# Performance work log

Hardware: AMD Instinct MI355X
Metric: run time of the kernel (lower is better)

## Reference

```python
import jax, jax.numpy as jnp
import numpy as np

LOC_SIZE, LOC_EMB = 100000, 256
TIM_SIZE, TIM_EMB = 48, 64
UID_SIZE, UID_EMB = 5000, 128
HID = 512
B, T = 64, 128
L_HIST, G = 1024, 4  # 256 history groups of size 4


def setup_inputs() -> dict:
    key = jax.random.key(0)
    ks = jax.random.split(key, 16)
    s = 0.02
    inp = {
        "loc": jax.random.randint(ks[0], (B, T), 0, LOC_SIZE),
        "tim": jax.random.randint(ks[1], (B, T), 0, TIM_SIZE),
        "input_lengths": jax.random.randint(ks[2], (B,), 1, T + 1),
        "history_loc": jax.random.randint(ks[3], (B, L_HIST), 0, LOC_SIZE),
        "history_tim": jax.random.randint(ks[4], (B, L_HIST), 0, TIM_SIZE),
        "history_uid": jax.random.randint(ks[5], (B, L_HIST), 0, UID_SIZE),
        "group_size": G,
        "emb_loc": jax.random.normal(ks[6], (LOC_SIZE, LOC_EMB), jnp.float32) * s,
        "emb_tim": jax.random.normal(ks[7], (TIM_SIZE, TIM_EMB), jnp.float32) * s,
        "emb_uid": jax.random.normal(ks[8], (UID_SIZE, UID_EMB), jnp.float32) * s,
        "W_attn": jax.random.normal(ks[9], (HID, LOC_EMB + TIM_EMB + UID_EMB), jnp.float32) * s,
        "b_attn": jnp.zeros((HID,), jnp.float32),
        "W_ih": jax.random.normal(ks[10], (3 * HID, LOC_EMB + TIM_EMB), jnp.float32) * s,
        "b_ih": jnp.zeros((3 * HID,), jnp.float32),
        "W_hh": jax.random.normal(ks[11], (3 * HID, HID), jnp.float32) * s,
        "b_hh": jnp.zeros((3 * HID,), jnp.float32),
        "W_final": jax.random.normal(ks[12], (UID_SIZE, 3 * HID), jnp.float32) * s,
        "b_final": jnp.zeros((UID_SIZE,), jnp.float32),
    }
    return inp


def _gru(x_seq, W_ih, b_ih, W_hh, b_hh):
    # x_seq: [T, B, Din] -> outputs [T, B, H], PyTorch gate order (r, z, n)
    H = W_hh.shape[1]
    gx = jnp.einsum("tbd,gd->tbg", x_seq, W_ih) + b_ih  # [T,B,3H]
    h0 = jnp.zeros((x_seq.shape[1], H), x_seq.dtype)

    def step(h, gx_t):
        gh = h @ W_hh.T + b_hh
        xr, xz, xn = jnp.split(gx_t, 3, axis=-1)
        hr, hz, hn = jnp.split(gh, 3, axis=-1)
        r = jax.nn.sigmoid(xr + hr)
        z = jax.nn.sigmoid(xz + hz)
        n = jnp.tanh(xn + r * hn)
        h_new = (1.0 - z) * n + z * h
        return h_new, h_new

    _, outs = jax.lax.scan(step, h0, gx)
    return outs  # [T,B,H]


def reference(loc, tim, input_lengths, history_loc, history_tim, history_uid,
              group_size, emb_loc, emb_tim, emb_uid, W_attn, b_attn,
              W_ih, b_ih, W_hh, b_hh, W_final, b_final):
    Bn, Tn = loc.shape
    # current-trajectory embeddings -> GRU (dropout is identity in eval)
    x = jnp.concatenate([emb_loc[loc], emb_tim[tim]], axis=-1)  # [B,T,Din]
    outs = _gru(jnp.swapaxes(x, 0, 1), W_ih, b_ih, W_hh, b_hh)  # [T,B,H]
    outs = jnp.swapaxes(outs, 0, 1)                              # [B,T,H]
    last = outs[jnp.arange(Bn), input_lengths - 1]               # [B,H]

    # history pooling: groups of size G; uid emb averaged within group,
    # loc/tim embeddings taken at each group's first element
    Gc = group_size
    n_groups = history_uid.shape[1] // Gc
    uid_h = emb_uid[history_uid].reshape(Bn, n_groups, Gc, -1).mean(axis=2)  # [B,N,Du]
    loc_h = emb_loc[history_loc[:, ::Gc]]                                    # [B,N,Dl]
    tim_h = emb_tim[history_tim[:, ::Gc]]                                    # [B,N,Dt]
    hist = jnp.concatenate([loc_h, tim_h, uid_h], axis=-1)
    hist = jnp.tanh(jnp.einsum("bnd,hd->bnh", hist, W_attn) + b_attn)        # [B,N,H]

    # 'dot' attention: replaces the nested python-loop scoring
    energies = jnp.einsum("bh,bnh->bn", last, hist)
    attn_w = jax.nn.softmax(energies, axis=-1)
    context = jnp.einsum("bn,bnh->bh", attn_w, hist)

    out = jnp.concatenate([last, context, last], axis=-1)  # [B,3H]
    y = out @ W_final.T + b_final                          # [B,U]
    # original assigns y (one row) into score[t] of shape [T,U] -> broadcast over T
    score = jnp.broadcast_to(y[:, None, :], (Bn, Tn, y.shape[-1]))
    return score
```

## Files before the change

### kernel.cpp

```cpp
#include <hip/hip_runtime.h>
#include <hip/hip_bf16.h>


typedef __attribute__((ext_vector_type(8))) short bf16x8;
typedef __attribute__((ext_vector_type(4))) float f32x4;
typedef __attribute__((ext_vector_type(4))) unsigned short u16x4;
typedef __attribute__((ext_vector_type(2))) unsigned long long u64x2;
typedef unsigned long long u64;

__device__ inline unsigned short f2bf(float x) {
  __hip_bfloat16 b = __float2bfloat16(x);
  return __builtin_bit_cast(unsigned short, b);
}
__device__ inline bf16x8 pack8(float4 a, float4 b) {
  bf16x8 w;
  w[0]=(short)f2bf(a.x); w[1]=(short)f2bf(a.y); w[2]=(short)f2bf(a.z); w[3]=(short)f2bf(a.w);
  w[4]=(short)f2bf(b.x); w[5]=(short)f2bf(b.y); w[6]=(short)f2bf(b.z); w[7]=(short)f2bf(b.w);
  return w;
}

__global__ __launch_bounds__(256)
void gemm_gx_f(const int* __restrict__ loc, const int* __restrict__ tim,
               const float* __restrict__ eloc, const float* __restrict__ etim,
               const float* __restrict__ W_ih, const float* __restrict__ b_ih,
               float* __restrict__ gx) {
  constexpr int LDR = 40, K = 320, N = 1536;
  __shared__ short Asl[128 * LDR];
  __shared__ short Bsl[128 * LDR];
  const int tid = threadIdx.x;
  const int lane = tid & 63, wid = tid >> 6;
  const int wr = wid >> 1, wc = wid & 1;
  const int m16 = lane & 15, g4 = lane >> 4;
  const int bm = blockIdx.y * 128, bn = blockIdx.x * 128;
  const int srow = tid >> 1, shalf = tid & 1;
  const int grow = bm + srow;
  const int t_ = grow >> 6, b_ = grow & 63;
  const float* aloc = eloc + (size_t)loc[b_ * 128 + t_] * 256 + (shalf << 4);
  const float* atim = etim + (size_t)tim[b_ * 128 + t_] * 64 + (shalf << 4);
  const float* bbase = W_ih + (size_t)(bn + srow) * K + (shalf << 4);
  float4 a0, a1, a2, a3, w0, w1, w2, w3;
  {
    a0 = ((const float4*)aloc)[0]; a1 = ((const float4*)aloc)[1];
    a2 = ((const float4*)aloc)[2]; a3 = ((const float4*)aloc)[3];
    w0 = ((const float4*)bbase)[0]; w1 = ((const float4*)bbase)[1];
    w2 = ((const float4*)bbase)[2]; w3 = ((const float4*)bbase)[3];
  }
  f32x4 acc[4][4] = {};
  for (int k0 = 0; k0 < K; k0 += 32) {
    short* arow = Asl + srow * LDR + (shalf << 4);
    *(bf16x8*)(arow)     = pack8(a0, a1);
    *(bf16x8*)(arow + 8) = pack8(a2, a3);
    short* brow = Bsl + srow * LDR + (shalf << 4);
    *(bf16x8*)(brow)     = pack8(w0, w1);
    *(bf16x8*)(brow + 8) = pack8(w2, w3);
    __syncthreads();
    if (k0 + 32 < K) {
      const int kn = k0 + 32;
      const float* ap = (kn < 256) ? (aloc + kn) : (atim + (kn - 256));
      a0 = ((const float4*)ap)[0]; a1 = ((const float4*)ap)[1];
      a2 = ((const float4*)ap)[2]; a3 = ((const float4*)ap)[3];
      const float* bp = bbase + kn;
      w0 = ((const float4*)bp)[0]; w1 = ((const float4*)bp)[1];
      w2 = ((const float4*)bp)[2]; w3 = ((const float4*)bp)[3];
    }
    bf16x8 af[4], bfr[4];
#pragma unroll
    for (int i = 0; i < 4; ++i) {
      af[i]  = *(const bf16x8*)(Asl + ((wr << 6) + (i << 4) + m16) * LDR + (g4 << 3));
      bfr[i] = *(const bf16x8*)(Bsl + ((wc << 6) + (i << 4) + m16) * LDR + (g4 << 3));
    }
#pragma unroll
    for (int i = 0; i < 4; ++i)
#pragma unroll
      for (int j = 0; j < 4; ++j)
        acc[i][j] = __builtin_amdgcn_mfma_f32_16x16x32_bf16(af[i], bfr[j], acc[i][j], 0, 0, 0);
    __syncthreads();
  }
#pragma unroll
  for (int i = 0; i < 4; ++i)
#pragma unroll
    for (int j = 0; j < 4; ++j) {
      const int col = bn + (wc << 6) + (j << 4) + m16;
      const float bv = b_ih[col];
#pragma unroll
      for (int q = 0; q < 4; ++q) {
        const int row = bm + (wr << 6) + (i << 4) + (g4 << 2) + q;
        gx[(size_t)row * N + col] = acc[i][j][q] + bv;
      }
    }
}

__global__ __launch_bounds__(256)
void gru_attn(const float* __restrict__ gx, const float* __restrict__ W_hh,
              const float* __restrict__ b_hh, const int* __restrict__ lens,
              short* __restrict__ h_bf, float* __restrict__ lastb,
              unsigned int* __restrict__ flags,
              const int* __restrict__ hloc, const int* __restrict__ htim,
              const int* __restrict__ huid,
              const float* __restrict__ eloc, const float* __restrict__ etim,
              const float* __restrict__ euid,
              const float* __restrict__ W_attn, const float* __restrict__ b_attn,
              float* __restrict__ histt, float* __restrict__ ctx) {
  __shared__ short smem[6 * 16 * 512];
  const int bid = blockIdx.x;
  const int tid = threadIdx.x;

  if (bid < 64) {
    if (tid >= 128) return;
    const int lane = tid & 63, tt = tid >> 6;
    const int c = bid >> 2, grp = bid & 3;
    const int j0 = (c << 5) + (tt << 4);
    const int b0 = grp << 4;
    const int m16 = lane & 15, g4 = lane >> 4;

    for (int gi = 0; gi < 3; ++gi) {
      const float* wg = W_hh + (size_t)(gi * 512 + j0) * 512;
      short* slab = smem + (((gi << 1) + tt) << 13);
      for (int r = 0; r < 16; ++r) {
        int k = lane << 3;
        const float4* src = (const float4*)(wg + (size_t)r * 512 + k);
        int off = ((r << 9) + k) ^ ((r & 7) << 3);
        *(bf16x8*)(slab + off) = pack8(src[0], src[1]);
      }
    }

    const int bcol = b0 + m16;
    const int jr = j0 + (g4 << 2);
    const f32x4 bhr = *(const f32x4*)&b_hh[jr];
    const f32x4 bhz = *(const f32x4*)&b_hh[512 + jr];
    const f32x4 bhn = *(const f32x4*)&b_hh[1024 + jr];
    const int lenb = lens[bcol];
    f32x4 hprev = {0.f, 0.f, 0.f, 0.f};

    unsigned int* gflags = flags + (grp << 9);
    unsigned int* ownflag = gflags + (((c << 1) + tt) << 4);

    for (int t = 0; t < 128; ++t) {
      const float* gxb = gx + ((size_t)t * 64 + bcol) * 1536;
      f32x4 gr = *(const f32x4*)(gxb + jr);
      f32x4 gz = *(const f32x4*)(gxb + 512 + jr);
      f32x4 gn = *(const f32x4*)(gxb + 1024 + jr);
      f32x4 ar = {0.f, 0.f, 0.f, 0.f}, az = ar, an = ar;
      if (t) {
        unsigned tgt = (unsigned)t;
        while (true) {
          unsigned f = tgt;
          if (lane < 32)
            f = __hip_atomic_load(gflags + (lane << 4), __ATOMIC_RELAXED, __HIP_MEMORY_SCOPE_AGENT);
          if (__all((int)(f >= tgt))) break;
        }
        asm volatile("" ::: "memory");

        const u64* hp = (const u64*)(h_bf + ((t & 1) << 15) + (size_t)bcol * 512 + (g4 << 3));
        u64 hu[32];
#pragma unroll
        for (int ks = 0; ks < 16; ++ks) {
          hu[2 * ks]     = __hip_atomic_load(hp + ks * 8,     __ATOMIC_RELAXED, __HIP_MEMORY_SCOPE_AGENT);
          hu[2 * ks + 1] = __hip_atomic_load(hp + ks * 8 + 1, __ATOMIC_RELAXED, __HIP_MEMORY_SCOPE_AGENT);
        }
#define GRU_MFMA(ks)                                                                 \
        {                                                                            \
          u64x2 p; p[0] = hu[2 * (ks)]; p[1] = hu[2 * (ks) + 1];                     \
          bf16x8 hf = __builtin_bit_cast(bf16x8, p);                                 \
          int off = ((m16 << 9) + ((ks) << 5) + (g4 << 3)) ^ ((m16 & 7) << 3);       \
          ar = __builtin_amdgcn_mfma_f32_16x16x32_bf16(*(const bf16x8*)(smem + ((0 + tt) << 13) + off), hf, ar, 0, 0, 0); \
          az = __builtin_amdgcn_mfma_f32_16x16x32_bf16(*(const bf16x8*)(smem + ((2 + tt) << 13) + off), hf, az, 0, 0, 0); \
          an = __builtin_amdgcn_mfma_f32_16x16x32_bf16(*(const bf16x8*)(smem + ((4 + tt) << 13) + off), hf, an, 0, 0, 0); \
        }
        GRU_MFMA(0)  GRU_MFMA(1)  GRU_MFMA(2)  GRU_MFMA(3)
        GRU_MFMA(4)  GRU_MFMA(5)  GRU_MFMA(6)  GRU_MFMA(7)
        GRU_MFMA(8)  GRU_MFMA(9)  GRU_MFMA(10) GRU_MFMA(11)
        GRU_MFMA(12) GRU_MFMA(13) GRU_MFMA(14) GRU_MFMA(15)
#undef GRU_MFMA
      }
      u16x4 hw;
#pragma unroll
      for (int q = 0; q < 4; ++q) {
        float r = 1.f / (1.f + __expf(-(gr[q] + ar[q] + bhr[q])));
        float z = 1.f / (1.f + __expf(-(gz[q] + az[q] + bhz[q])));
        float xn = gn[q] + r * (an[q] + bhn[q]);
        float n = 1.f - 2.f / (__expf(2.f * xn) + 1.f);
        float hv = (1.f - z) * n + z * hprev[q];
        hprev[q] = hv;
        hw[q] = f2bf(hv);
      }
      __hip_atomic_store((u64*)(h_bf + ((~t & 1) << 15) + (size_t)bcol * 512 + jr),
                         __builtin_bit_cast(u64, hw),
                         __ATOMIC_RELAXED, __HIP_MEMORY_SCOPE_AGENT);
      if (t == lenb - 1) {
        *(f32x4*)(lastb + (size_t)bcol * 512 + jr) = hprev;
      }
      if (t < 127) {
        asm volatile("s_waitcnt vmcnt(0)" ::: "memory");
        if (lane == 0)
          __hip_atomic_store(ownflag, (unsigned)(t + 1), __ATOMIC_RELAXED, __HIP_MEMORY_SCOPE_AGENT);
      }
    }
    asm volatile("s_waitcnt vmcnt(0)" ::: "memory");
    if (lane == 0)
      __hip_atomic_fetch_add(flags + 2064, 1u, __ATOMIC_RELEASE, __HIP_MEMORY_SCOPE_AGENT);
    return;
  }

  {
    constexpr int LDR = 40, K = 448, N = 512;
    short* Asl = smem;
    short* Bsl = smem + 128 * LDR;
    const int lane = tid & 63, wid = tid >> 6;
    const int wr = wid >> 1, wc = wid & 1;
    const int m16 = lane & 15, g4 = lane >> 4;
    const int srow = tid >> 1, shalf = tid & 1;
    for (int tile = bid - 64; tile < 512; tile += 128) {
      const int yt = tile >> 2, nt = tile & 3;
      const int bm = yt << 7, bn = nt << 7;
      f32x4 acc[4][4] = {};
      for (int k0 = 0; k0 < K; k0 += 32) {
        {
          const int grow = bm + srow;
          const int b = grow >> 8, n = grow & 255;
          const int base = b * 1024 + (n << 2);
          float4 f0, f1, f2, f3;
          if (k0 < 256) {
            const float* ap = eloc + (size_t)hloc[base] * 256 + k0 + (shalf << 4);
            f0 = ((const float4*)ap)[0]; f1 = ((const float4*)ap)[1];
            f2 = ((const float4*)ap)[2]; f3 = ((const float4*)ap)[3];
          } else if (k0 < 320) {
            const float* ap = etim + (size_t)htim[base] * 64 + (k0 - 256) + (shalf << 4);
            f0 = ((const float4*)ap)[0]; f1 = ((const float4*)ap)[1];
            f2 = ((const float4*)ap)[2]; f3 = ((const float4*)ap)[3];
          } else {
            const int cu = (k0 - 320) + (shalf << 4);
            const float4* u0 = (const float4*)(euid + (size_t)huid[base + 0] * 128 + cu);
            const float4* u1 = (const float4*)(euid + (size_t)huid[base + 1] * 128 + cu);
            const float4* u2 = (const float4*)(euid + (size_t)huid[base + 2] * 128 + cu);
            const float4* u3 = (const float4*)(euid + (size_t)huid[base + 3] * 128 + cu);
#define AVG4(idx, dst) { float4 a=u0[idx],b4=u1[idx],c4=u2[idx],d4=u3[idx];            \
            dst.x=0.25f*(a.x+b4.x+c4.x+d4.x); dst.y=0.25f*(a.y+b4.y+c4.y+d4.y);       \
            dst.z=0.25f*(a.z+b4.z+c4.z+d4.z); dst.w=0.25f*(a.w+b4.w+c4.w+d4.w); }
            AVG4(0, f0) AVG4(1, f1) AVG4(2, f2) AVG4(3, f3)
#undef AVG4
          }
          short* arow = Asl + srow * LDR + (shalf << 4);
          *(bf16x8*)(arow)     = pack8(f0, f1);
          *(bf16x8*)(arow + 8) = pack8(f2, f3);
          const float* bp = W_attn + (size_t)(bn + srow) * K + k0 + (shalf << 4);
          f0 = ((const float4*)bp)[0]; f1 = ((const float4*)bp)[1];
          f2 = ((const float4*)bp)[2]; f3 = ((const float4*)bp)[3];
          short* brow = Bsl + srow * LDR + (shalf << 4);
          *(bf16x8*)(brow)     = pack8(f0, f1);
          *(bf16x8*)(brow + 8) = pack8(f2, f3);
        }
        __syncthreads();
        bf16x8 af[4], bfr[4];
#pragma unroll
        for (int i = 0; i < 4; ++i) {
          af[i]  = *(const bf16x8*)(Asl + ((wr << 6) + (i << 4) + m16) * LDR + (g4 << 3));
          bfr[i] = *(const bf16x8*)(Bsl + ((wc << 6) + (i << 4) + m16) * LDR + (g4 << 3));
        }
#pragma unroll
        for (int i = 0; i < 4; ++i)
#pragma unroll
          for (int j = 0; j < 4; ++j)
            acc[i][j] = __builtin_amdgcn_mfma_f32_16x16x32_bf16(af[i], bfr[j], acc[i][j], 0, 0, 0);
        __syncthreads();
      }
#pragma unroll
      for (int i = 0; i < 4; ++i)
#pragma unroll
        for (int j = 0; j < 4; ++j) {
          const int col = bn + (wc << 6) + (j << 4) + m16;
          const float bv = b_attn[col];
#pragma unroll
          for (int q = 0; q < 4; ++q) {
            const int row = bm + (wr << 6) + (i << 4) + (g4 << 2) + q;
            histt[(size_t)row * N + col] = tanhf(acc[i][j][q] + bv);
          }
        }
    }
    asm volatile("s_waitcnt vmcnt(0)" ::: "memory");
    if (tid == 0)
      __hip_atomic_fetch_add(flags + 2048, 1u, __ATOMIC_RELEASE, __HIP_MEMORY_SCOPE_AGENT);
  }

  if (bid < 128) {
    while (true) {
      unsigned a = __hip_atomic_load(flags + 2048, __ATOMIC_RELAXED, __HIP_MEMORY_SCOPE_AGENT);
      unsigned g = __hip_atomic_load(flags + 2064, __ATOMIC_RELAXED, __HIP_MEMORY_SCOPE_AGENT);
      if (a >= 128u && g >= 128u) break;
      __builtin_amdgcn_s_sleep(2);
    }
    __builtin_amdgcn_fence(__ATOMIC_ACQUIRE, "agent");
    __syncthreads();
    const int b = bid - 64;
    float* ls  = (float*)smem;
    float* wv  = ls + 512;
    float* red = wv + 256;
    ((float2*)ls)[tid] = ((const float2*)(lastb + (size_t)b * 512))[tid];
    __syncthreads();
    const float* hb = histt + (size_t)b * 256 * 512;
    const float* hrow = hb + (size_t)tid * 512;
    float acc = 0.f;
    for (int k = 0; k < 512; k += 4) {
      float4 h4 = *(const float4*)(hrow + k);
      acc += ls[k] * h4.x + ls[k + 1] * h4.y + ls[k + 2] * h4.z + ls[k + 3] * h4.w;
    }
    red[tid] = acc;
    __syncthreads();
    for (int s = 128; s; s >>= 1) {
      if (tid < s) red[tid] = fmaxf(red[tid], red[tid + s]);
      __syncthreads();
    }
    float m = red[0];
    __syncthreads();
    float ex = expf(acc - m);
    wv[tid] = ex; red[tid] = ex;
    __syncthreads();
    for (int s = 128; s; s >>= 1) {
      if (tid < s) red[tid] += red[tid + s];
      __syncthreads();
    }
    float inv = 1.f / red[0];
    float c0 = 0.f, c1 = 0.f;
    for (int n = 0; n < 256; ++n) {
      float wn = wv[n];
      c0 += wn * hb[(size_t)n * 512 + tid];
      c1 += wn * hb[(size_t)n * 512 + tid + 256];
    }
    ctx[(size_t)b * 512 + tid]       = c0 * inv;
    ctx[(size_t)b * 512 + tid + 256] = c1 * inv;
  }
}

__global__ __launch_bounds__(256)
void final_gemm(const float* __restrict__ last, const float* __restrict__ ctx,
                const float* __restrict__ Wf, const float* __restrict__ bf,
                float* __restrict__ y) {
  __shared__ float s[64][132];
  const int tid = threadIdx.x;
  const int u0 = blockIdx.x << 3;
  const int ul = tid >> 6, b = tid & 63;
  float acc0 = 0.f, acc1 = 0.f;
  for (int kc = 0; kc < 12; ++kc) {
    __syncthreads();
    for (int i = tid; i < 2048; i += 256) {
      int rb = i >> 5, cc = (i & 31) << 2;
      int k = kc * 128 + cc;
      const float* src = (k < 512) ? (last + (size_t)rb * 512 + k)
                       : (k < 1024) ? (ctx + (size_t)rb * 512 + k - 512)
                                    : (last + (size_t)rb * 512 + k - 1024);
      *(float4*)&s[rb][cc] = *(const float4*)src;
    }
    __syncthreads();
#pragma unroll
    for (int uu = 0; uu < 2; ++uu) {
      int u = u0 + ul + uu * 4;
      const float* wrow = Wf + (size_t)u * 1536 + kc * 128;
      float a = 0.f;
#pragma unroll 8
      for (int c = 0; c < 128; c += 4) {
        float4 w4 = *(const float4*)(wrow + c);
        float4 s4 = *(const float4*)&s[b][c];
        a += w4.x * s4.x + w4.y * s4.y + w4.z * s4.z + w4.w * s4.w;
      }
      if (uu == 0) acc0 += a; else acc1 += a;
    }
  }
  int u = u0 + ul;
  y[(size_t)b * 5000 + u]     = acc0 + bf[u];
  y[(size_t)b * 5000 + u + 4] = acc1 + bf[u + 4];
}

__global__ void broadcast_y(const float* __restrict__ y, float* __restrict__ out) {
  int bt = blockIdx.x;
  const float4* src = (const float4*)(y + (size_t)(bt >> 7) * 5000);
  float4* dst = (float4*)(out + (size_t)bt * 5000);
  for (int i = threadIdx.x; i < 1250; i += 256) dst[i] = src[i];
}

extern "C" void kernel_launch(void* const* d_in, const int* in_sizes, int n_in,
                              void* d_out, int out_size, void* d_ws, size_t ws_size,
                              hipStream_t stream) {
  const int* loc  = (const int*)d_in[0];
  const int* tim  = (const int*)d_in[1];
  const int* lens = (const int*)d_in[2];
  const int* hloc = (const int*)d_in[3];
  const int* htim = (const int*)d_in[4];
  const int* huid = (const int*)d_in[5];
  const float* eloc    = (const float*)d_in[7];
  const float* etim    = (const float*)d_in[8];
  const float* euid    = (const float*)d_in[9];
  const float* W_attn  = (const float*)d_in[10];
  const float* b_attn  = (const float*)d_in[11];
  const float* W_ih    = (const float*)d_in[12];
  const float* b_ih    = (const float*)d_in[13];
  const float* W_hh    = (const float*)d_in[14];
  const float* b_hh    = (const float*)d_in[15];
  const float* W_final = (const float*)d_in[16];
  const float* b_final = (const float*)d_in[17];
  float* out = (float*)d_out;
  char* ws = (char*)d_ws;

  float* gx    = (float*)(ws + 0ull);
  float* histt = (float*)(ws + 50331648ull);
  float* lastb = (float*)(ws + 83886080ull);
  float* ctx   = (float*)(ws + 84017152ull);
  float* yv    = (float*)(ws + 84148224ull);
  short* h_bf  = (short*)(ws + 85428224ull);
  unsigned int* flags = (unsigned int*)(ws + 85559296ull);

  hipMemsetAsync(flags, 0, 12288, stream);
  gemm_gx_f<<<dim3(12, 64), 256, 0, stream>>>(loc, tim, eloc, etim, W_ih, b_ih, gx);

  gru_attn<<<192, 256, 0, stream>>>(gx, W_hh, b_hh, lens, h_bf, lastb, flags,
                                    hloc, htim, huid, eloc, etim, euid,
                                    W_attn, b_attn, histt, ctx);

  final_gemm<<<625, 256, 0, stream>>>(lastb, ctx, W_final, b_final, yv);
  broadcast_y<<<8192, 256, 0, stream>>>(yv, out);
}
```

Before: 672.4 us.

## Repartition GRU across 32 four-wave blocks and fold duplicated W_final columns

The recurrent GRU part now runs on 32 blocks of four waves instead of 64 blocks of two. Each block covers 64 hidden units, which cuts the number of cross-block flags polled per step from 32 to 8. The n-gate W_hh slice is kept in registers and the r/z slices in LDS, and waves in a block sync with __syncthreads before publishing the step flag. The history-attention blocks, while waiting, also precompute W_final[:, :512] + W_final[:, 1024:], since `last` appears twice in the concatenation. This lets final_gemm read a K of 1024 instead of 1536. The added block barrier per step and the extra register pressure could lengthen each serial step.

```diff
diff --git a/kernel.cpp b/kernel.cpp
--- a/kernel.cpp
+++ b/kernel.cpp
@@ -90,7 +90,7 @@
     }
 }
 
-__global__ __launch_bounds__(256)
+__global__ __launch_bounds__(256, 1)
 void gru_attn(const float* __restrict__ gx, const float* __restrict__ W_hh,
               const float* __restrict__ b_hh, const int* __restrict__ lens,
               short* __restrict__ h_bf, float* __restrict__ lastb,
@@ -100,27 +100,37 @@
               const float* __restrict__ eloc, const float* __restrict__ etim,
               const float* __restrict__ euid,
               const float* __restrict__ W_attn, const float* __restrict__ b_attn,
+              const float* __restrict__ Wf, float* __restrict__ Wfold,
               float* __restrict__ histt, float* __restrict__ ctx) {
-  __shared__ short smem[6 * 16 * 512];
+  __shared__ short smem[8 * 16 * 512];
   const int bid = blockIdx.x;
   const int tid = threadIdx.x;
 
-  if (bid < 64) {
-    if (tid >= 128) return;
-    const int lane = tid & 63, tt = tid >> 6;
+  if (bid < 32) {
+    const int lane = tid & 63, w = tid >> 6;
     const int c = bid >> 2, grp = bid & 3;
-    const int j0 = (c << 5) + (tt << 4);
+    const int j0 = (c << 6) + (w << 4);
     const int b0 = grp << 4;
     const int m16 = lane & 15, g4 = lane >> 4;
 
-    for (int gi = 0; gi < 3; ++gi) {
+    for (int gi = 0; gi < 2; ++gi) {
       const float* wg = W_hh + (size_t)(gi * 512 + j0) * 512;
-      short* slab = smem + (((gi << 1) + tt) << 13);
+      short* slab = smem + (((w << 1) + gi) << 13);
       for (int r = 0; r < 16; ++r) {
         int k = lane << 3;
         const float4* src = (const float4*)(wg + (size_t)r * 512 + k);
         int off = ((r << 9) + k) ^ ((r & 7) << 3);
         *(bf16x8*)(slab + off) = pack8(src[0], src[1]);
+      }
+    }
+    bf16x8 wn_[16];
+    {
+      const float* wnp = W_hh + (size_t)(1024 + j0 + m16) * 512 + (g4 << 3);
+#pragma unroll
+      for (int ks = 0; ks < 16; ++ks) {
+        float4 x0 = *(const float4*)(wnp + ks * 32);
+        float4 x1 = *(const float4*)(wnp + ks * 32 + 4);
+        wn_[ks] = pack8(x0, x1);
       }
     }
 
@@ -132,8 +142,8 @@
     const int lenb = lens[bcol];
     f32x4 hprev = {0.f, 0.f, 0.f, 0.f};
 
-    unsigned int* gflags = flags + (grp << 9);
-    unsigned int* ownflag = gflags + (((c << 1) + tt) << 4);
+    unsigned int* gflags = flags + (grp << 7);
+    unsigned int* ownflag = gflags + (c << 4);
 
     for (int t = 0; t < 128; ++t) {
       const float* gxb = gx + ((size_t)t * 64 + bcol) * 1536;
@@ -145,7 +155,7 @@
         unsigned tgt = (unsigned)t;
         while (true) {
           unsigned f = tgt;
-          if (lane < 32)
+          if (lane < 8)
             f = __hip_atomic_load(gflags + (lane << 4), __ATOMIC_RELAXED, __HIP_MEMORY_SCOPE_AGENT);
           if (__all((int)(f >= tgt))) break;
         }
@@ -163,9 +173,9 @@
           u64x2 p; p[0] = hu[2 * (ks)]; p[1] = hu[2 * (ks) + 1];                     \
           bf16x8 hf = __builtin_bit_cast(bf16x8, p);                                 \
           int off = ((m16 << 9) + ((ks) << 5) + (g4 << 3)) ^ ((m16 & 7) << 3);       \
-          ar = __builtin_amdgcn_mfma_f32_16x16x32_bf16(*(const bf16x8*)(smem + ((0 + tt) << 13) + off), hf, ar, 0, 0, 0); \
-          az = __builtin_amdgcn_mfma_f32_16x16x32_bf16(*(const bf16x8*)(smem + ((2 + tt) << 13) + off), hf, az, 0, 0, 0); \
-          an = __builtin_amdgcn_mfma_f32_16x16x32_bf16(*(const bf16x8*)(smem + ((4 + tt) << 13) + off), hf, an, 0, 0, 0); \
+          ar = __builtin_amdgcn_mfma_f32_16x16x32_bf16(*(const bf16x8*)(smem + ((w << 1) << 13) + off), hf, ar, 0, 0, 0);       \
+          az = __builtin_amdgcn_mfma_f32_16x16x32_bf16(*(const bf16x8*)(smem + (((w << 1) + 1) << 13) + off), hf, az, 0, 0, 0); \
+          an = __builtin_amdgcn_mfma_f32_16x16x32_bf16(wn_[ks], hf, an, 0, 0, 0);    \
         }
         GRU_MFMA(0)  GRU_MFMA(1)  GRU_MFMA(2)  GRU_MFMA(3)
         GRU_MFMA(4)  GRU_MFMA(5)  GRU_MFMA(6)  GRU_MFMA(7)
@@ -192,12 +202,14 @@
       }
       if (t < 127) {
         asm volatile("s_waitcnt vmcnt(0)" ::: "memory");
-        if (lane == 0)
+        __syncthreads();
+        if (tid == 0)
           __hip_atomic_store(ownflag, (unsigned)(t + 1), __ATOMIC_RELAXED, __HIP_MEMORY_SCOPE_AGENT);
       }
     }
     asm volatile("s_waitcnt vmcnt(0)" ::: "memory");
-    if (lane == 0)
+    __syncthreads();
+    if (tid == 0)
       __hip_atomic_fetch_add(flags + 2064, 1u, __ATOMIC_RELEASE, __HIP_MEMORY_SCOPE_AGENT);
     return;
   }
@@ -210,7 +222,7 @@
     const int wr = wid >> 1, wc = wid & 1;
     const int m16 = lane & 15, g4 = lane >> 4;
     const int srow = tid >> 1, shalf = tid & 1;
-    for (int tile = bid - 64; tile < 512; tile += 128) {
+    for (int tile = bid - 32; tile < 512; tile += 128) {
       const int yt = tile >> 2, nt = tile & 3;
       const int bm = yt << 7, bn = nt << 7;
       f32x4 acc[4][4] = {};
@@ -280,18 +292,28 @@
     asm volatile("s_waitcnt vmcnt(0)" ::: "memory");
     if (tid == 0)
       __hip_atomic_fetch_add(flags + 2048, 1u, __ATOMIC_RELEASE, __HIP_MEMORY_SCOPE_AGENT);
-  }
-
-  if (bid < 128) {
-    while (true) {
-      unsigned a = __hip_atomic_load(flags + 2048, __ATOMIC_RELAXED, __HIP_MEMORY_SCOPE_AGENT);
-      unsigned g = __hip_atomic_load(flags + 2064, __ATOMIC_RELAXED, __HIP_MEMORY_SCOPE_AGENT);
-      if (a >= 128u && g >= 128u) break;
-      __builtin_amdgcn_s_sleep(2);
-    }
+
+    for (int u = bid - 32; u < 5000; u += 128) {
+      const int cc = tid << 1;
+      float2 a = *(const float2*)(Wf + (size_t)u * 1536 + cc);
+      float2 b2 = *(const float2*)(Wf + (size_t)u * 1536 + 1024 + cc);
+      float2 o; o.x = a.x + b2.x; o.y = a.y + b2.y;
+      *(float2*)(Wfold + (size_t)u * 512 + cc) = o;
+    }
+  }
+
+  if (bid < 96) {
+    if (tid == 0) {
+      while (true) {
+        unsigned a = __hip_atomic_load(flags + 2048, __ATOMIC_RELAXED, __HIP_MEMORY_SCOPE_AGENT);
+        unsigned g = __hip_atomic_load(flags + 2064, __ATOMIC_RELAXED, __HIP_MEMORY_SCOPE_AGENT);
+        if (a >= 128u && g >= 32u) break;
+        __builtin_amdgcn_s_sleep(7);
+      }
+    }
+    __syncthreads();
     __builtin_amdgcn_fence(__ATOMIC_ACQUIRE, "agent");
-    __syncthreads();
-    const int b = bid - 64;
+    const int b = bid - 32;
     float* ls  = (float*)smem;
     float* wv  = ls + 512;
     float* red = wv + 256;
@@ -333,28 +355,28 @@
 
 __global__ __launch_bounds__(256)
 void final_gemm(const float* __restrict__ last, const float* __restrict__ ctx,
-                const float* __restrict__ Wf, const float* __restrict__ bf,
-                float* __restrict__ y) {
+                const float* __restrict__ Wfold, const float* __restrict__ Wf,
+                const float* __restrict__ bf, float* __restrict__ y) {
   __shared__ float s[64][132];
   const int tid = threadIdx.x;
   const int u0 = blockIdx.x << 3;
   const int ul = tid >> 6, b = tid & 63;
   float acc0 = 0.f, acc1 = 0.f;
-  for (int kc = 0; kc < 12; ++kc) {
+  for (int kc = 0; kc < 8; ++kc) {
     __syncthreads();
     for (int i = tid; i < 2048; i += 256) {
       int rb = i >> 5, cc = (i & 31) << 2;
       int k = kc * 128 + cc;
       const float* src = (k < 512) ? (last + (size_t)rb * 512 + k)
-                       : (k < 1024) ? (ctx + (size_t)rb * 512 + k - 512)
-                                    : (last + (size_t)rb * 512 + k - 1024);
+                                   : (ctx + (size_t)rb * 512 + k - 512);
       *(float4*)&s[rb][cc] = *(const float4*)src;
     }
     __syncthreads();
 #pragma unroll
     for (int uu = 0; uu < 2; ++uu) {
       int u = u0 + ul + uu * 4;
-      const float* wrow = Wf + (size_t)u * 1536 + kc * 128;
+      const float* wrow = (kc < 4) ? (Wfold + (size_t)u * 512 + kc * 128)
+                                   : (Wf + (size_t)u * 1536 + 512 + (kc - 4) * 128);
       float a = 0.f;
 #pragma unroll 8
       for (int c = 0; c < 128; c += 4) {
@@ -407,14 +429,15 @@
   float* yv    = (float*)(ws + 84148224ull);
   short* h_bf  = (short*)(ws + 85428224ull);
   unsigned int* flags = (unsigned int*)(ws + 85559296ull);
+  float* Wfold = (float*)(ws + 85571584ull);
 
   hipMemsetAsync(flags, 0, 12288, stream);
   gemm_gx_f<<<dim3(12, 64), 256, 0, stream>>>(loc, tim, eloc, etim, W_ih, b_ih, gx);
 
-  gru_attn<<<192, 256, 0, stream>>>(gx, W_hh, b_hh, lens, h_bf, lastb, flags,
+  gru_attn<<<160, 256, 0, stream>>>(gx, W_hh, b_hh, lens, h_bf, lastb, flags,
                                     hloc, htim, huid, eloc, etim, euid,
-                                    W_attn, b_attn, histt, ctx);
-
-  final_gemm<<<625, 256, 0, stream>>>(lastb, ctx, W_final, b_final, yv);
+                                    W_attn, b_attn, W_final, Wfold, histt, ctx);
+
+  final_gemm<<<625, 256, 0, stream>>>(lastb, ctx, Wfold, W_final, b_final, yv);
   broadcast_y<<<8192, 256, 0, stream>>>(yv, out);
 }
```

New measurement: 851.5 us. +26.6%, slower.

## Fold duplicated last-state weight columns and sync GRU block pairs with one flag

Applied to the files above, without the earlier changes.

Because the final input is [last, ctx, last], the attention blocks now precompute Wfold = W_final[:, :512] + W_final[:, 1024:], which shrinks the final GEMM's K from 1536 to 1024. The GRU recurrence now merges its two waves' progress flags into one per block, synchronized with __syncthreads. Idle waves loop through matching barriers, and consumers poll fewer flags. The waiting blocks also poll with a single thread and a longer sleep. The costs are a folding pass over W_final done inside the GRU-overlapped phase and an extra block barrier on every recurrence step.

```diff
diff --git a/kernel.cpp b/kernel.cpp
--- a/kernel.cpp
+++ b/kernel.cpp
@@ -100,13 +100,17 @@
               const float* __restrict__ eloc, const float* __restrict__ etim,
               const float* __restrict__ euid,
               const float* __restrict__ W_attn, const float* __restrict__ b_attn,
+              const float* __restrict__ Wf, float* __restrict__ Wfold,
               float* __restrict__ histt, float* __restrict__ ctx) {
   __shared__ short smem[6 * 16 * 512];
   const int bid = blockIdx.x;
   const int tid = threadIdx.x;
 
   if (bid < 64) {
-    if (tid >= 128) return;
+    if (tid >= 128) {
+      for (int t = 0; t < 128; ++t) __syncthreads();
+      return;
+    }
     const int lane = tid & 63, tt = tid >> 6;
     const int c = bid >> 2, grp = bid & 3;
     const int j0 = (c << 5) + (tt << 4);
@@ -123,6 +127,7 @@
         *(bf16x8*)(slab + off) = pack8(src[0], src[1]);
       }
     }
+    __syncthreads();
 
     const int bcol = b0 + m16;
     const int jr = j0 + (g4 << 2);
@@ -132,8 +137,8 @@
     const int lenb = lens[bcol];
     f32x4 hprev = {0.f, 0.f, 0.f, 0.f};
 
-    unsigned int* gflags = flags + (grp << 9);
-    unsigned int* ownflag = gflags + (((c << 1) + tt) << 4);
+    unsigned int* gflags = flags + (grp << 8);
+    unsigned int* ownflag = gflags + (c << 4);
 
     for (int t = 0; t < 128; ++t) {
       const float* gxb = gx + ((size_t)t * 64 + bcol) * 1536;
@@ -145,7 +150,7 @@
         unsigned tgt = (unsigned)t;
         while (true) {
           unsigned f = tgt;
-          if (lane < 32)
+          if (lane < 16)
             f = __hip_atomic_load(gflags + (lane << 4), __ATOMIC_RELAXED, __HIP_MEMORY_SCOPE_AGENT);
           if (__all((int)(f >= tgt))) break;
         }
@@ -192,7 +197,8 @@
       }
       if (t < 127) {
         asm volatile("s_waitcnt vmcnt(0)" ::: "memory");
-        if (lane == 0)
+        __syncthreads();
+        if (tid == 0)
           __hip_atomic_store(ownflag, (unsigned)(t + 1), __ATOMIC_RELAXED, __HIP_MEMORY_SCOPE_AGENT);
       }
     }
@@ -280,17 +286,27 @@
     asm volatile("s_waitcnt vmcnt(0)" ::: "memory");
     if (tid == 0)
       __hip_atomic_fetch_add(flags + 2048, 1u, __ATOMIC_RELEASE, __HIP_MEMORY_SCOPE_AGENT);
+
+    for (int u = bid - 64; u < 5000; u += 128) {
+      const int cc = tid << 1;
+      float2 a = *(const float2*)(Wf + (size_t)u * 1536 + cc);
+      float2 b2 = *(const float2*)(Wf + (size_t)u * 1536 + 1024 + cc);
+      float2 o; o.x = a.x + b2.x; o.y = a.y + b2.y;
+      *(float2*)(Wfold + (size_t)u * 512 + cc) = o;
+    }
   }
 
   if (bid < 128) {
-    while (true) {
-      unsigned a = __hip_atomic_load(flags + 2048, __ATOMIC_RELAXED, __HIP_MEMORY_SCOPE_AGENT);
-      unsigned g = __hip_atomic_load(flags + 2064, __ATOMIC_RELAXED, __HIP_MEMORY_SCOPE_AGENT);
-      if (a >= 128u && g >= 128u) break;
-      __builtin_amdgcn_s_sleep(2);
-    }
+    if (tid == 0) {
+      while (true) {
+        unsigned a = __hip_atomic_load(flags + 2048, __ATOMIC_RELAXED, __HIP_MEMORY_SCOPE_AGENT);
+        unsigned g = __hip_atomic_load(flags + 2064, __ATOMIC_RELAXED, __HIP_MEMORY_SCOPE_AGENT);
+        if (a >= 128u && g >= 128u) break;
+        __builtin_amdgcn_s_sleep(7);
+      }
+    }
+    __syncthreads();
     __builtin_amdgcn_fence(__ATOMIC_ACQUIRE, "agent");
-    __syncthreads();
     const int b = bid - 64;
     float* ls  = (float*)smem;
     float* wv  = ls + 512;
@@ -333,28 +349,28 @@
 
 __global__ __launch_bounds__(256)
 void final_gemm(const float* __restrict__ last, const float* __restrict__ ctx,
-                const float* __restrict__ Wf, const float* __restrict__ bf,
-                float* __restrict__ y) {
+                const float* __restrict__ Wfold, const float* __restrict__ Wf,
+                const float* __restrict__ bf, float* __restrict__ y) {
   __shared__ float s[64][132];
   const int tid = threadIdx.x;
   const int u0 = blockIdx.x << 3;
   const int ul = tid >> 6, b = tid & 63;
   float acc0 = 0.f, acc1 = 0.f;
-  for (int kc = 0; kc < 12; ++kc) {
+  for (int kc = 0; kc < 8; ++kc) {
     __syncthreads();
     for (int i = tid; i < 2048; i += 256) {
       int rb = i >> 5, cc = (i & 31) << 2;
       int k = kc * 128 + cc;
       const float* src = (k < 512) ? (last + (size_t)rb * 512 + k)
-                       : (k < 1024) ? (ctx + (size_t)rb * 512 + k - 512)
-                                    : (last + (size_t)rb * 512 + k - 1024);
+                                   : (ctx + (size_t)rb * 512 + k - 512);
       *(float4*)&s[rb][cc] = *(const float4*)src;
     }
     __syncthreads();
 #pragma unroll
     for (int uu = 0; uu < 2; ++uu) {
       int u = u0 + ul + uu * 4;
-      const float* wrow = Wf + (size_t)u * 1536 + kc * 128;
+      const float* wrow = (kc < 4) ? (Wfold + (size_t)u * 512 + kc * 128)
+                                   : (Wf + (size_t)u * 1536 + 512 + (kc - 4) * 128);
       float a = 0.f;
 #pragma unroll 8
       for (int c = 0; c < 128; c += 4) {
@@ -407,14 +423,15 @@
   float* yv    = (float*)(ws + 84148224ull);
   short* h_bf  = (short*)(ws + 85428224ull);
   unsigned int* flags = (unsigned int*)(ws + 85559296ull);
+  float* Wfold = (float*)(ws + 85571584ull);
 
   hipMemsetAsync(flags, 0, 12288, stream);
   gemm_gx_f<<<dim3(12, 64), 256, 0, stream>>>(loc, tim, eloc, etim, W_ih, b_ih, gx);
 
   gru_attn<<<192, 256, 0, stream>>>(gx, W_hh, b_hh, lens, h_bf, lastb, flags,
                                     hloc, htim, huid, eloc, etim, euid,
-                                    W_attn, b_attn, histt, ctx);
-
-  final_gemm<<<625, 256, 0, stream>>>(lastb, ctx, W_final, b_final, yv);
+                                    W_attn, b_attn, W_final, Wfold, histt, ctx);
+
+  final_gemm<<<625, 256, 0, stream>>>(lastb, ctx, Wfold, W_final, b_final, yv);
   broadcast_y<<<8192, 256, 0, stream>>>(yv, out);
 }
```

Result: faster. 616.6 us (-8.3%).
